# Kernel optimization log

Hardware: AMD Instinct MI355X
Metric: run time of the kernel (lower is better)

## Reference

```python
import jax, jax.numpy as jnp
import numpy as np

SEQ = 21  # fixed by bias parameter shape in the original module

def setup_inputs() -> dict:
    key = jax.random.key(0)
    ks = jax.random.split(key, 6)
    B, H = 8192, 1024
    stdv = 1.0 / np.sqrt(H)
    return {
        "c": jax.random.normal(ks[0], (1, B, H), dtype=jnp.float32),
        "allh": jax.random.normal(ks[1], (SEQ, B, H), dtype=jnp.float32),
        "W": jax.random.uniform(ks[2], (H, H), jnp.float32, -stdv, stdv),
        "V": jax.random.uniform(ks[3], (H, H), jnp.float32, -stdv, stdv),
        "bias": jax.random.uniform(ks[4], (SEQ, H), jnp.float32, -stdv, stdv),
        "Wt": jax.random.uniform(ks[5], (H, 1), jnp.float32, -stdv, stdv),
    }

def reference(c, allh, W, V, bias, Wt):
    # c: [1, B, H] -> [B, 1, H]; allh: [S, B, H] -> [B, S, H]
    c_b = jnp.transpose(c, (1, 0, 2))
    h_b = jnp.transpose(allh, (1, 0, 2))
    wc = jnp.einsum('boh,hk->bok', c_b, W)          # [B, 1, H], broadcasts over S
    vh = jnp.einsum('bsh,hk->bsk', h_b, V)          # [B, S, H]
    e = jnp.tanh(wc + vh + bias)                    # [B, S, H]
    scores = jnp.einsum('bsh,ho->bso', e, Wt)       # [B, S, 1]
    alpha = jax.nn.softmax(scores, axis=1)          # softmax over seq axis
    y = jnp.sum(alpha * h_b, axis=1, keepdims=True) # [B, 1, H]
    return jnp.transpose(y, (1, 0, 2))              # [1, B, H]
```

## Files before the change

kernel.cpp:

```cpp
#include <hip/hip_runtime.h>
#include <hip/hip_bf16.h>
#include <cstdint>
#include <cstddef>

#define Bq 8192
#define Sq 21
#define Hq 1024
#define Mq (Bq * Sq)

typedef __attribute__((ext_vector_type(8))) short short8;
typedef __attribute__((ext_vector_type(4))) float floatx4;

__device__ __forceinline__ short f2b(float x) {
    unsigned u = __builtin_bit_cast(unsigned, x);
    unsigned r = (u + 0x7fffu + ((u >> 16) & 1u)) >> 16;
    return (short)r;
}
__device__ __forceinline__ float b2f(unsigned short b) {
    return __builtin_bit_cast(float, (unsigned)b << 16);
}

__device__ __forceinline__ void gl_lds16(const void* g, void* l) {
    __builtin_amdgcn_global_load_lds(
        (const __attribute__((address_space(1))) unsigned int*)g,
        (__attribute__((address_space(3))) unsigned int*)l, 16, 0, 0);
}

__global__ void transpose_cvt(const float* __restrict__ src,
                              unsigned short* __restrict__ dst) {
    __shared__ float tile[32][33];
    const int n0 = blockIdx.x * 32;
    const int k0 = blockIdx.y * 32;
    const int tx = threadIdx.x;
    const int ty = threadIdx.y;
    #pragma unroll
    for (int i = ty; i < 32; i += 8)
        tile[i][tx] = src[(size_t)(k0 + i) * Hq + n0 + tx];
    __syncthreads();
    #pragma unroll
    for (int i = ty; i < 32; i += 8)
        dst[(size_t)(n0 + i) * Hq + k0 + tx] = (unsigned short)f2b(tile[tx][i]);
}

__global__ __launch_bounds__(256) void cvt_bf16(const float* __restrict__ src,
                                                unsigned short* __restrict__ dst,
                                                int n8) {
    int i = blockIdx.x * 256 + threadIdx.x;
    const int stride = gridDim.x * 256;
    for (; i < n8; i += stride) {
        const float4* s4 = reinterpret_cast<const float4*>(src) + (size_t)i * 2;
        float4 a = s4[0], b = s4[1];
        short8 p;
        p[0] = f2b(a.x); p[1] = f2b(a.y); p[2] = f2b(a.z); p[3] = f2b(a.w);
        p[4] = f2b(b.x); p[5] = f2b(b.y); p[6] = f2b(b.z); p[7] = f2b(b.w);
        reinterpret_cast<short8*>(dst)[i] = p;
    }
}

__global__ __launch_bounds__(256, 3) void gemm_wc2(
    const unsigned short* __restrict__ cb, const unsigned short* __restrict__ Wtr,
    float* __restrict__ wc)
{
    __shared__ unsigned short As[128 * 64];
    __shared__ unsigned short Bs[128 * 64];

    const int n0 = blockIdx.x * 128;
    const int m0 = blockIdx.y * 128;
    const int t = threadIdx.x;
    const int lane = t & 63;
    const int w = t >> 6;

    const int sub = lane >> 3;
    const int k8g = (lane & 7) ^ sub;
    const unsigned short* ap[4];
    const unsigned short* bp[4];
    #pragma unroll
    for (int j = 0; j < 4; ++j) {
        const int r = w * 32 + j * 8 + sub;
        ap[j] = cb + (size_t)(m0 + r) * Hq + k8g * 8;
        bp[j] = Wtr + (size_t)(n0 + r) * Hq + k8g * 8;
    }

    const int wm = (w & 1) * 64;
    const int wn = (w >> 1) * 64;
    const int l15 = lane & 15;
    const int q = lane >> 4;
    const int sw = l15 & 7;

    floatx4 acc[4][4] = {};
    const short8* AsV = (const short8*)As;
    const short8* BsV = (const short8*)Bs;

    for (int k0 = 0; k0 < Hq; k0 += 64) {
        __syncthreads();
        #pragma unroll
        for (int j = 0; j < 4; ++j) {
            gl_lds16(ap[j] + k0, &As[(w * 256 + j * 64) * 8]);
            gl_lds16(bp[j] + k0, &Bs[(w * 256 + j * 64) * 8]);
        }
        __syncthreads();
        #pragma unroll
        for (int kk = 0; kk < 2; ++kk) {
            const int k8 = kk * 4 + q;
            short8 af[4], bfr[4];
            #pragma unroll
            for (int i = 0; i < 4; ++i) {
                af[i]  = AsV[((wm + i * 16 + l15) << 3) | (k8 ^ sw)];
                bfr[i] = BsV[((wn + i * 16 + l15) << 3) | (k8 ^ sw)];
            }
            #pragma unroll
            for (int i = 0; i < 4; ++i)
                #pragma unroll
                for (int j = 0; j < 4; ++j)
                    acc[i][j] = __builtin_amdgcn_mfma_f32_16x16x32_bf16(
                        af[i], bfr[j], acc[i][j], 0, 0, 0);
        }
    }

    #pragma unroll
    for (int i = 0; i < 4; ++i)
        #pragma unroll
        for (int rr = 0; rr < 4; ++rr) {
            const int mm = m0 + wm + i * 16 + q * 4 + rr;
            #pragma unroll
            for (int j = 0; j < 4; ++j) {
                const int nn = n0 + wn + j * 16 + l15;
                wc[(size_t)mm * Hq + nn] = acc[i][j][rr];
            }
        }
}

__global__ __launch_bounds__(256, 3) void gemm_scores2(
    const unsigned short* __restrict__ hb, const unsigned short* __restrict__ Vt,
    const float* __restrict__ wc, const float* __restrict__ bias,
    const float* __restrict__ Wt, float* __restrict__ scores)
{
    __shared__ unsigned short As[128 * 64];
    __shared__ unsigned short Bs[128 * 64];

    const int n0 = blockIdx.x * 128;
    const int m0 = blockIdx.y * 128;
    const int t = threadIdx.x;
    const int lane = t & 63;
    const int w = t >> 6;

    const int sub = lane >> 3;
    const int k8g = (lane & 7) ^ sub;
    const unsigned short* ap[4];
    const unsigned short* bp[4];
    #pragma unroll
    for (int j = 0; j < 4; ++j) {
        const int r = w * 32 + j * 8 + sub;
        const int m = m0 + r;
        const int bb = m / 21;
        const int ss = m - bb * 21;
        ap[j] = hb + ((size_t)ss * Bq + bb) * Hq + k8g * 8;
        bp[j] = Vt + (size_t)(n0 + r) * Hq + k8g * 8;
    }

    const int wm = (w & 1) * 64;
    const int wn = (w >> 1) * 64;
    const int l15 = lane & 15;
    const int q = lane >> 4;
    const int sw = l15 & 7;

    floatx4 acc[4][4] = {};
    const short8* AsV = (const short8*)As;
    const short8* BsV = (const short8*)Bs;

    for (int k0 = 0; k0 < Hq; k0 += 64) {
        __syncthreads();
        #pragma unroll
        for (int j = 0; j < 4; ++j) {
            gl_lds16(ap[j] + k0, &As[(w * 256 + j * 64) * 8]);
            gl_lds16(bp[j] + k0, &Bs[(w * 256 + j * 64) * 8]);
        }
        __syncthreads();
        #pragma unroll
        for (int kk = 0; kk < 2; ++kk) {
            const int k8 = kk * 4 + q;
            short8 af[4], bfr[4];
            #pragma unroll
            for (int i = 0; i < 4; ++i) {
                af[i]  = AsV[((wm + i * 16 + l15) << 3) | (k8 ^ sw)];
                bfr[i] = BsV[((wn + i * 16 + l15) << 3) | (k8 ^ sw)];
            }
            #pragma unroll
            for (int i = 0; i < 4; ++i)
                #pragma unroll
                for (int j = 0; j < 4; ++j)
                    acc[i][j] = __builtin_amdgcn_mfma_f32_16x16x32_bf16(
                        af[i], bfr[j], acc[i][j], 0, 0, 0);
        }
    }

    float wtv[4];
    #pragma unroll
    for (int j = 0; j < 4; ++j) wtv[j] = Wt[n0 + wn + j * 16 + l15];

    #pragma unroll
    for (int i = 0; i < 4; ++i) {
        #pragma unroll
        for (int rr = 0; rr < 4; ++rr) {
            const int mm = m0 + wm + i * 16 + q * 4 + rr;
            const int b2 = mm / 21;
            const int s2 = mm - b2 * 21;
            const float* wcrow = wc + (size_t)b2 * Hq + n0 + wn;
            const float* birow = bias + (size_t)s2 * Hq + n0 + wn;
            float part = 0.f;
            #pragma unroll
            for (int j = 0; j < 4; ++j) {
                const int nl = j * 16 + l15;
                float e = tanhf(acc[i][j][rr] + wcrow[nl] + birow[nl]);
                part += e * wtv[j];
            }
            part += __shfl_xor(part, 1);
            part += __shfl_xor(part, 2);
            part += __shfl_xor(part, 4);
            part += __shfl_xor(part, 8);
            if (l15 == 0) atomicAdd(&scores[mm], part);
        }
    }
}

__global__ __launch_bounds__(256) void softmax_out2(
    const float* __restrict__ scores, const unsigned short* __restrict__ hb,
    float* __restrict__ out)
{
    const int b = blockIdx.x;
    const int t = threadIdx.x;

    float sc[Sq];
    float mx = -1e30f;
    #pragma unroll
    for (int s = 0; s < Sq; ++s) {
        sc[s] = scores[(size_t)b * Sq + s];
        mx = fmaxf(mx, sc[s]);
    }
    float sum = 0.f;
    #pragma unroll
    for (int s = 0; s < Sq; ++s) {
        sc[s] = __expf(sc[s] - mx);
        sum += sc[s];
    }
    const float inv = 1.0f / sum;

    const int h = t * 4;
    float a0 = 0.f, a1 = 0.f, a2 = 0.f, a3 = 0.f;
    #pragma unroll
    for (int s = 0; s < Sq; ++s) {
        const unsigned short* p = hb + ((size_t)s * Bq + b) * Hq + h;
        uint2 u = *reinterpret_cast<const uint2*>(p);
        a0 += sc[s] * b2f((unsigned short)(u.x & 0xffffu));
        a1 += sc[s] * b2f((unsigned short)(u.x >> 16));
        a2 += sc[s] * b2f((unsigned short)(u.y & 0xffffu));
        a3 += sc[s] * b2f((unsigned short)(u.y >> 16));
    }
    float4 r;
    r.x = a0 * inv; r.y = a1 * inv; r.z = a2 * inv; r.w = a3 * inv;
    *reinterpret_cast<float4*>(out + (size_t)b * Hq + h) = r;
}

__global__ __launch_bounds__(256, 2) void gemm_wc_fb(
    const float* __restrict__ c, const unsigned short* __restrict__ Wtr,
    float* __restrict__ wc)
{
    __shared__ short As[128][72];
    __shared__ short Bs[128][72];
    const int m0 = blockIdx.x * 128;
    const int n0 = blockIdx.y * 128;
    const int t = threadIdx.x;
    const int r = t >> 1;
    const int half = t & 1;
    const float*          arow = c + (size_t)(m0 + r) * Hq + half * 32;
    const unsigned short* brow = Wtr + (size_t)(n0 + r) * Hq + half * 32;
    const int lane = t & 63;
    const int w = t >> 6;
    const int wm = (w & 1) * 64;
    const int wn = (w >> 1) * 64;
    const int l15 = lane & 15;
    const int q = lane >> 4;
    floatx4 acc[4][4] = {};
    for (int k0 = 0; k0 < Hq; k0 += 64) {
        __syncthreads();
        const float4* a4 = reinterpret_cast<const float4*>(arow + k0);
        #pragma unroll
        for (int i = 0; i < 4; ++i) {
            float4 v0 = a4[2 * i], v1 = a4[2 * i + 1];
            short8 p;
            p[0] = f2b(v0.x); p[1] = f2b(v0.y); p[2] = f2b(v0.z); p[3] = f2b(v0.w);
            p[4] = f2b(v1.x); p[5] = f2b(v1.y); p[6] = f2b(v1.z); p[7] = f2b(v1.w);
            *reinterpret_cast<short8*>(&As[r][half * 32 + i * 8]) = p;
        }
        const short8* b8 = reinterpret_cast<const short8*>(brow + k0);
        #pragma unroll
        for (int i = 0; i < 4; ++i)
            *reinterpret_cast<short8*>(&Bs[r][half * 32 + i * 8]) = b8[i];
        __syncthreads();
        #pragma unroll
        for (int kk = 0; kk < 64; kk += 32) {
            short8 af[4], bfr[4];
            #pragma unroll
            for (int i = 0; i < 4; ++i)
                af[i] = *reinterpret_cast<const short8*>(&As[wm + i * 16 + l15][kk + q * 8]);
            #pragma unroll
            for (int j = 0; j < 4; ++j)
                bfr[j] = *reinterpret_cast<const short8*>(&Bs[wn + j * 16 + l15][kk + q * 8]);
            #pragma unroll
            for (int i = 0; i < 4; ++i)
                #pragma unroll
                for (int j = 0; j < 4; ++j)
                    acc[i][j] = __builtin_amdgcn_mfma_f32_16x16x32_bf16(
                        af[i], bfr[j], acc[i][j], 0, 0, 0);
        }
    }
    #pragma unroll
    for (int i = 0; i < 4; ++i)
        #pragma unroll
        for (int rr = 0; rr < 4; ++rr) {
            const int mm = m0 + wm + i * 16 + q * 4 + rr;
            #pragma unroll
            for (int j = 0; j < 4; ++j)
                wc[(size_t)mm * Hq + n0 + wn + j * 16 + l15] = acc[i][j][rr];
        }
}

__global__ __launch_bounds__(256, 2) void gemm_scores_fb(
    const float* __restrict__ allh, const unsigned short* __restrict__ Vt,
    const float* __restrict__ wc, const float* __restrict__ bias,
    const float* __restrict__ Wt, float* __restrict__ scores)
{
    __shared__ short As[128][72];
    __shared__ short Bs[128][72];
    const int m0 = blockIdx.x * 128;
    const int n0 = blockIdx.y * 128;
    const int t = threadIdx.x;
    const int r = t >> 1;
    const int half = t & 1;
    const int m = m0 + r;
    const int bb = m / 21;
    const int ss = m - bb * 21;
    const float* arow = allh + (size_t)ss * (Bq * Hq) + (size_t)bb * Hq + half * 32;
    const unsigned short* brow = Vt + (size_t)(n0 + r) * Hq + half * 32;
    const int lane = t & 63;
    const int w = t >> 6;
    const int wm = (w & 1) * 64;
    const int wn = (w >> 1) * 64;
    const int l15 = lane & 15;
    const int q = lane >> 4;
    floatx4 acc[4][4] = {};
    for (int k0 = 0; k0 < Hq; k0 += 64) {
        __syncthreads();
        const float4* a4 = reinterpret_cast<const float4*>(arow + k0);
        #pragma unroll
        for (int i = 0; i < 4; ++i) {
            float4 v0 = a4[2 * i], v1 = a4[2 * i + 1];
            short8 p;
            p[0] = f2b(v0.x); p[1] = f2b(v0.y); p[2] = f2b(v0.z); p[3] = f2b(v0.w);
            p[4] = f2b(v1.x); p[5] = f2b(v1.y); p[6] = f2b(v1.z); p[7] = f2b(v1.w);
            *reinterpret_cast<short8*>(&As[r][half * 32 + i * 8]) = p;
        }
        const short8* b8 = reinterpret_cast<const short8*>(brow + k0);
        #pragma unroll
        for (int i = 0; i < 4; ++i)
            *reinterpret_cast<short8*>(&Bs[r][half * 32 + i * 8]) = b8[i];
        __syncthreads();
        #pragma unroll
        for (int kk = 0; kk < 64; kk += 32) {
            short8 af[4], bfr[4];
            #pragma unroll
            for (int i = 0; i < 4; ++i)
                af[i] = *reinterpret_cast<const short8*>(&As[wm + i * 16 + l15][kk + q * 8]);
            #pragma unroll
            for (int j = 0; j < 4; ++j)
                bfr[j] = *reinterpret_cast<const short8*>(&Bs[wn + j * 16 + l15][kk + q * 8]);
            #pragma unroll
            for (int i = 0; i < 4; ++i)
                #pragma unroll
                for (int j = 0; j < 4; ++j)
                    acc[i][j] = __builtin_amdgcn_mfma_f32_16x16x32_bf16(
                        af[i], bfr[j], acc[i][j], 0, 0, 0);
        }
    }
    float wtv[4];
    #pragma unroll
    for (int j = 0; j < 4; ++j) wtv[j] = Wt[n0 + wn + j * 16 + l15];
    #pragma unroll
    for (int i = 0; i < 4; ++i)
        #pragma unroll
        for (int rr = 0; rr < 4; ++rr) {
            const int mm = m0 + wm + i * 16 + q * 4 + rr;
            const int b2 = mm / 21;
            const int s2 = mm - b2 * 21;
            const float* wcrow = wc + (size_t)b2 * Hq + n0 + wn;
            const float* birow = bias + (size_t)s2 * Hq + n0 + wn;
            float part = 0.f;
            #pragma unroll
            for (int j = 0; j < 4; ++j) {
                const int nl = j * 16 + l15;
                float e = tanhf(acc[i][j][rr] + wcrow[nl] + birow[nl]);
                part += e * wtv[j];
            }
            part += __shfl_xor(part, 1);
            part += __shfl_xor(part, 2);
            part += __shfl_xor(part, 4);
            part += __shfl_xor(part, 8);
            if (l15 == 0) atomicAdd(&scores[mm], part);
        }
}

__global__ __launch_bounds__(256) void softmax_out_fb(
    const float* __restrict__ scores, const float* __restrict__ allh,
    float* __restrict__ out)
{
    const int b = blockIdx.x;
    const int t = threadIdx.x;
    float sc[Sq];
    float mx = -1e30f;
    #pragma unroll
    for (int s = 0; s < Sq; ++s) {
        sc[s] = scores[(size_t)b * Sq + s];
        mx = fmaxf(mx, sc[s]);
    }
    float sum = 0.f;
    #pragma unroll
    for (int s = 0; s < Sq; ++s) {
        sc[s] = __expf(sc[s] - mx);
        sum += sc[s];
    }
    const float inv = 1.0f / sum;
    for (int h = t; h < Hq; h += 256) {
        float acc = 0.f;
        #pragma unroll
        for (int s = 0; s < Sq; ++s)
            acc += sc[s] * allh[(size_t)s * (Bq * Hq) + (size_t)b * Hq + h];
        out[(size_t)b * Hq + h] = acc * inv;
    }
}

extern "C" void kernel_launch(void* const* d_in, const int* in_sizes, int n_in,
                              void* d_out, int out_size, void* d_ws, size_t ws_size,
                              hipStream_t stream) {
    const float* c    = (const float*)d_in[0];
    const float* allh = (const float*)d_in[1];
    const float* W    = (const float*)d_in[2];
    const float* V    = (const float*)d_in[3];
    const float* bias = (const float*)d_in[4];
    const float* Wt   = (const float*)d_in[5];
    float* out = (float*)d_out;
    char* ws = (char*)d_ws;

    const size_t NEED = 411041792ULL;

    if (ws_size >= NEED) {
        unsigned short* Vt  = (unsigned short*)ws;
        unsigned short* Wtr = (unsigned short*)(ws + 2097152);
        float* wc           = (float*)(ws + 4194304);
        float* scores       = (float*)(ws + 37748736);
        unsigned short* cb  = (unsigned short*)(ws + 41943040);
        unsigned short* hb  = (unsigned short*)(ws + 58720256);

        hipMemsetAsync(scores, 0, (size_t)Bq * Sq * sizeof(float), stream);
        transpose_cvt<<<dim3(32, 32), dim3(32, 8), 0, stream>>>(W, Wtr);
        transpose_cvt<<<dim3(32, 32), dim3(32, 8), 0, stream>>>(V, Vt);
        cvt_bf16<<<1024, 256, 0, stream>>>(c, cb, Bq * Hq / 8);
        cvt_bf16<<<4096, 256, 0, stream>>>(allh, hb, Sq * (Bq / 8) * Hq);

        gemm_wc2<<<dim3(Hq / 128, Bq / 128), 256, 0, stream>>>(cb, Wtr, wc);
        gemm_scores2<<<dim3(Hq / 128, Mq / 128), 256, 0, stream>>>(
            hb, Vt, wc, bias, Wt, scores);
        softmax_out2<<<Bq, 256, 0, stream>>>(scores, hb, out);
    } else {
        unsigned short* Vt  = (unsigned short*)ws;
        unsigned short* Wtr = (unsigned short*)(ws + (2u << 20));
        float* wc     = (float*)(ws + (4u << 20));
        float* scores = (float*)(ws + (4u << 20) + (size_t)Bq * Hq * 4);

        hipMemsetAsync(scores, 0, (size_t)Bq * Sq * sizeof(float), stream);
        transpose_cvt<<<dim3(32, 32), dim3(32, 8), 0, stream>>>(W, Wtr);
        transpose_cvt<<<dim3(32, 32), dim3(32, 8), 0, stream>>>(V, Vt);
        gemm_wc_fb<<<dim3(Bq / 128, Hq / 128), 256, 0, stream>>>(c, Wtr, wc);
        gemm_scores_fb<<<dim3(Mq / 128, Hq / 128), 256, 0, stream>>>(
            allh, Vt, wc, bias, Wt, scores);
        softmax_out_fb<<<Bq, 256, 0, stream>>>(scores, allh, out);
    }
}
```

Measured before the change: 1.854 ms.

## Use 256x256 double-buffered tiles with block swizzle and fast tanh in scores GEMM

Replaces the 128x128 scores GEMM with a 256x256 tile, 512-thread kernel where each wave computes 128x64. Global-to-LDS loads are double-buffered so the next K-slice streams in while the current one is multiplied, and the flat grid is swizzled across 8 groups for better L2 locality. tanhf is replaced by an exp/rcp approximation. The larger tile raises register pressure and LDS use (128KB), which limits occupancy, and the fast tanh slightly changes accuracy.

```diff
diff --git a/kernel.cpp b/kernel.cpp
--- a/kernel.cpp
+++ b/kernel.cpp
@@ -18,6 +18,11 @@
 }
 __device__ __forceinline__ float b2f(unsigned short b) {
     return __builtin_bit_cast(float, (unsigned)b << 16);
+}
+
+__device__ __forceinline__ float fast_tanh(float x) {
+    float e = __expf(2.0f * x);
+    return fmaf(-2.0f, __builtin_amdgcn_rcpf(e + 1.0f), 1.0f);
 }
 
 __device__ __forceinline__ void gl_lds16(const void* g, void* l) {
@@ -130,16 +135,57 @@
         }
 }
 
-__global__ __launch_bounds__(256, 3) void gemm_scores2(
+__device__ __forceinline__ void stage_step(
+    unsigned short* __restrict__ buf, int w,
+    const unsigned short* const (&ap)[4], const unsigned short* const (&bp)[4],
+    int k0)
+{
+    unsigned short* dstA = buf + w * 2048;
+    unsigned short* dstB = buf + 16384 + w * 2048;
+    #pragma unroll
+    for (int j = 0; j < 4; ++j) {
+        gl_lds16(ap[j] + k0, dstA + j * 512);
+        gl_lds16(bp[j] + k0, dstB + j * 512);
+    }
+}
+
+__device__ __forceinline__ void compute_step(
+    const unsigned short* __restrict__ buf,
+    floatx4 (&acc)[8][4], int wm, int wn, int l15, int q, int sw)
+{
+    const short8* AsV = (const short8*)buf;
+    const short8* BsV = (const short8*)(buf + 16384);
+    #pragma unroll
+    for (int kk = 0; kk < 2; ++kk) {
+        const int k8 = kk * 4 + q;
+        short8 af[8], bfv[4];
+        #pragma unroll
+        for (int i = 0; i < 8; ++i)
+            af[i] = AsV[((wm + i * 16 + l15) << 3) | (k8 ^ sw)];
+        #pragma unroll
+        for (int j = 0; j < 4; ++j)
+            bfv[j] = BsV[((wn + j * 16 + l15) << 3) | (k8 ^ sw)];
+        #pragma unroll
+        for (int i = 0; i < 8; ++i)
+            #pragma unroll
+            for (int j = 0; j < 4; ++j)
+                acc[i][j] = __builtin_amdgcn_mfma_f32_16x16x32_bf16(
+                    af[i], bfv[j], acc[i][j], 0, 0, 0);
+    }
+}
+
+__global__ __launch_bounds__(512, 2) void gemm_scores256(
     const unsigned short* __restrict__ hb, const unsigned short* __restrict__ Vt,
     const float* __restrict__ wc, const float* __restrict__ bias,
     const float* __restrict__ Wt, float* __restrict__ scores)
 {
-    __shared__ unsigned short As[128 * 64];
-    __shared__ unsigned short Bs[128 * 64];
-
-    const int n0 = blockIdx.x * 128;
-    const int m0 = blockIdx.y * 128;
+    __shared__ unsigned short lds[65536];
+
+    const int orig = blockIdx.x;
+    const int swz = (orig & 7) * 336 + (orig >> 3);
+    const int n0 = (swz & 3) * 256;
+    const int m0 = (swz >> 2) * 256;
+
     const int t = threadIdx.x;
     const int lane = t & 63;
     const int w = t >> 6;
@@ -158,39 +204,31 @@
         bp[j] = Vt + (size_t)(n0 + r) * Hq + k8g * 8;
     }
 
-    const int wm = (w & 1) * 64;
-    const int wn = (w >> 1) * 64;
+    const int wm = (w >> 2) * 128;
+    const int wn = (w & 3) * 64;
     const int l15 = lane & 15;
     const int q = lane >> 4;
     const int sw = l15 & 7;
 
-    floatx4 acc[4][4] = {};
-    const short8* AsV = (const short8*)As;
-    const short8* BsV = (const short8*)Bs;
-
-    for (int k0 = 0; k0 < Hq; k0 += 64) {
-        __syncthreads();
-        #pragma unroll
-        for (int j = 0; j < 4; ++j) {
-            gl_lds16(ap[j] + k0, &As[(w * 256 + j * 64) * 8]);
-            gl_lds16(bp[j] + k0, &Bs[(w * 256 + j * 64) * 8]);
-        }
-        __syncthreads();
-        #pragma unroll
-        for (int kk = 0; kk < 2; ++kk) {
-            const int k8 = kk * 4 + q;
-            short8 af[4], bfr[4];
-            #pragma unroll
-            for (int i = 0; i < 4; ++i) {
-                af[i]  = AsV[((wm + i * 16 + l15) << 3) | (k8 ^ sw)];
-                bfr[i] = BsV[((wn + i * 16 + l15) << 3) | (k8 ^ sw)];
-            }
-            #pragma unroll
-            for (int i = 0; i < 4; ++i)
-                #pragma unroll
-                for (int j = 0; j < 4; ++j)
-                    acc[i][j] = __builtin_amdgcn_mfma_f32_16x16x32_bf16(
-                        af[i], bfr[j], acc[i][j], 0, 0, 0);
+    floatx4 acc[8][4] = {};
+
+    unsigned short* buf0 = lds;
+    unsigned short* buf1 = lds + 32768;
+
+    stage_step(buf0, w, ap, bp, 0);
+    __syncthreads();
+
+    #pragma unroll 1
+    for (int tt = 0; tt < 8; ++tt) {
+        stage_step(buf1, w, ap, bp, tt * 128 + 64);
+        compute_step(buf0, acc, wm, wn, l15, q, sw);
+        __syncthreads();
+        if (tt < 7) {
+            stage_step(buf0, w, ap, bp, tt * 128 + 128);
+            compute_step(buf1, acc, wm, wn, l15, q, sw);
+            __syncthreads();
+        } else {
+            compute_step(buf1, acc, wm, wn, l15, q, sw);
         }
     }
 
@@ -199,7 +237,7 @@
     for (int j = 0; j < 4; ++j) wtv[j] = Wt[n0 + wn + j * 16 + l15];
 
     #pragma unroll
-    for (int i = 0; i < 4; ++i) {
+    for (int i = 0; i < 8; ++i) {
         #pragma unroll
         for (int rr = 0; rr < 4; ++rr) {
             const int mm = m0 + wm + i * 16 + q * 4 + rr;
@@ -211,7 +249,7 @@
             #pragma unroll
             for (int j = 0; j < 4; ++j) {
                 const int nl = j * 16 + l15;
-                float e = tanhf(acc[i][j][rr] + wcrow[nl] + birow[nl]);
+                float e = fast_tanh(acc[i][j][rr] + wcrow[nl] + birow[nl]);
                 part += e * wtv[j];
             }
             part += __shfl_xor(part, 1);
@@ -467,7 +505,7 @@
         cvt_bf16<<<4096, 256, 0, stream>>>(allh, hb, Sq * (Bq / 8) * Hq);
 
         gemm_wc2<<<dim3(Hq / 128, Bq / 128), 256, 0, stream>>>(cb, Wtr, wc);
-        gemm_scores2<<<dim3(Hq / 128, Mq / 128), 256, 0, stream>>>(
+        gemm_scores256<<<dim3((Mq / 256) * (Hq / 256)), dim3(512), 0, stream>>>(
             hb, Vt, wc, bias, Wt, scores);
         softmax_out2<<<Bq, 256, 0, stream>>>(scores, hb, out);
     } else {
```

Result: slower. 3.037 ms (+63.8%).

## Double-buffer LDS in scores GEMM, swizzle block order, use fast tanh

Applied to the files above, without the earlier changes.

The main scores GEMM now uses two LDS buffers so that global-to-LDS loads for the next K tile overlap MFMA compute on the current one, which halves the barriers per tile. The launch becomes a 1D grid whose block index is remapped so that blocks scheduled together share A tiles, aiming at better L2 reuse. The precise tanhf is replaced with an exp/rcp approximation to cut epilogue cost. Doubling LDS use lowers occupancy (launch bounds drop from 3 to 2 blocks per CU), and the fast tanh gives up some accuracy.

```diff
diff --git a/kernel.cpp b/kernel.cpp
--- a/kernel.cpp
+++ b/kernel.cpp
@@ -18,6 +18,11 @@
 }
 __device__ __forceinline__ float b2f(unsigned short b) {
     return __builtin_bit_cast(float, (unsigned)b << 16);
+}
+
+__device__ __forceinline__ float fast_tanh(float x) {
+    float e = __expf(2.0f * x);
+    return fmaf(-2.0f, __builtin_amdgcn_rcpf(e + 1.0f), 1.0f);
 }
 
 __device__ __forceinline__ void gl_lds16(const void* g, void* l) {
@@ -130,16 +135,56 @@
         }
 }
 
-__global__ __launch_bounds__(256, 3) void gemm_scores2(
+__device__ __forceinline__ void stage128(
+    unsigned short* __restrict__ bufA, int w,
+    const unsigned short* const (&ap)[4], const unsigned short* const (&bp)[4],
+    int k0)
+{
+    unsigned short* dstA = bufA + w * 2048;
+    unsigned short* dstB = bufA + 8192 + w * 2048;
+    #pragma unroll
+    for (int j = 0; j < 4; ++j) {
+        gl_lds16(ap[j] + k0, dstA + j * 512);
+        gl_lds16(bp[j] + k0, dstB + j * 512);
+    }
+}
+
+__device__ __forceinline__ void compute128(
+    const unsigned short* __restrict__ bufA,
+    floatx4 (&acc)[4][4], int wm, int wn, int l15, int q, int sw)
+{
+    const short8* AsV = (const short8*)bufA;
+    const short8* BsV = (const short8*)(bufA + 8192);
+    #pragma unroll
+    for (int kk = 0; kk < 2; ++kk) {
+        const int k8 = kk * 4 + q;
+        short8 af[4], bfr[4];
+        #pragma unroll
+        for (int i = 0; i < 4; ++i) {
+            af[i]  = AsV[((wm + i * 16 + l15) << 3) | (k8 ^ sw)];
+            bfr[i] = BsV[((wn + i * 16 + l15) << 3) | (k8 ^ sw)];
+        }
+        #pragma unroll
+        for (int i = 0; i < 4; ++i)
+            #pragma unroll
+            for (int j = 0; j < 4; ++j)
+                acc[i][j] = __builtin_amdgcn_mfma_f32_16x16x32_bf16(
+                    af[i], bfr[j], acc[i][j], 0, 0, 0);
+    }
+}
+
+__global__ __launch_bounds__(256, 2) void gemm_scores128db(
     const unsigned short* __restrict__ hb, const unsigned short* __restrict__ Vt,
     const float* __restrict__ wc, const float* __restrict__ bias,
     const float* __restrict__ Wt, float* __restrict__ scores)
 {
-    __shared__ unsigned short As[128 * 64];
-    __shared__ unsigned short Bs[128 * 64];
-
-    const int n0 = blockIdx.x * 128;
-    const int m0 = blockIdx.y * 128;
+    __shared__ unsigned short lds[32768];
+
+    const int orig = blockIdx.x;
+    const int swz = (orig & 7) * 1344 + (orig >> 3);
+    const int n0 = (swz & 7) * 128;
+    const int m0 = (swz >> 3) * 128;
+
     const int t = threadIdx.x;
     const int lane = t & 63;
     const int w = t >> 6;
@@ -165,32 +210,24 @@
     const int sw = l15 & 7;
 
     floatx4 acc[4][4] = {};
-    const short8* AsV = (const short8*)As;
-    const short8* BsV = (const short8*)Bs;
-
-    for (int k0 = 0; k0 < Hq; k0 += 64) {
-        __syncthreads();
-        #pragma unroll
-        for (int j = 0; j < 4; ++j) {
-            gl_lds16(ap[j] + k0, &As[(w * 256 + j * 64) * 8]);
-            gl_lds16(bp[j] + k0, &Bs[(w * 256 + j * 64) * 8]);
-        }
-        __syncthreads();
-        #pragma unroll
-        for (int kk = 0; kk < 2; ++kk) {
-            const int k8 = kk * 4 + q;
-            short8 af[4], bfr[4];
-            #pragma unroll
-            for (int i = 0; i < 4; ++i) {
-                af[i]  = AsV[((wm + i * 16 + l15) << 3) | (k8 ^ sw)];
-                bfr[i] = BsV[((wn + i * 16 + l15) << 3) | (k8 ^ sw)];
-            }
-            #pragma unroll
-            for (int i = 0; i < 4; ++i)
-                #pragma unroll
-                for (int j = 0; j < 4; ++j)
-                    acc[i][j] = __builtin_amdgcn_mfma_f32_16x16x32_bf16(
-                        af[i], bfr[j], acc[i][j], 0, 0, 0);
+
+    unsigned short* buf0 = lds;
+    unsigned short* buf1 = lds + 16384;
+
+    stage128(buf0, w, ap, bp, 0);
+    __syncthreads();
+
+    #pragma unroll 1
+    for (int tt = 0; tt < 8; ++tt) {
+        stage128(buf1, w, ap, bp, tt * 128 + 64);
+        compute128(buf0, acc, wm, wn, l15, q, sw);
+        __syncthreads();
+        if (tt < 7) {
+            stage128(buf0, w, ap, bp, tt * 128 + 128);
+            compute128(buf1, acc, wm, wn, l15, q, sw);
+            __syncthreads();
+        } else {
+            compute128(buf1, acc, wm, wn, l15, q, sw);
         }
     }
 
@@ -211,7 +248,7 @@
             #pragma unroll
             for (int j = 0; j < 4; ++j) {
                 const int nl = j * 16 + l15;
-                float e = tanhf(acc[i][j][rr] + wcrow[nl] + birow[nl]);
+                float e = fast_tanh(acc[i][j][rr] + wcrow[nl] + birow[nl]);
                 part += e * wtv[j];
             }
             part += __shfl_xor(part, 1);
@@ -467,7 +504,7 @@
         cvt_bf16<<<4096, 256, 0, stream>>>(allh, hb, Sq * (Bq / 8) * Hq);
 
         gemm_wc2<<<dim3(Hq / 128, Bq / 128), 256, 0, stream>>>(cb, Wtr, wc);
-        gemm_scores2<<<dim3(Hq / 128, Mq / 128), 256, 0, stream>>>(
+        gemm_scores128db<<<dim3((Mq / 128) * (Hq / 128)), 256, 0, stream>>>(
             hb, Vt, wc, bias, Wt, scores);
         softmax_out2<<<Bq, 256, 0, stream>>>(scores, hb, out);
     } else {
```

New measurement: 1.725 ms. 1.07x faster.

## Triple-buffer scores GEMM with 512-thread 128x256 tiles and fast tanh

Applied to the files above, without the earlier changes.

Replaces the scores GEMM with a 512-thread block computing 128x256 tiles. Global-to-LDS loads for A and B go through a three-stage LDS ring, so loads for step k+2 are in flight while step k computes, with one barrier per step and MFMA priority raised. It also adds a block-index swizzle for L2 locality and swaps tanhf for an exp/rcp approximation. The risks are one block per CU (lower occupancy), the larger LDS footprint, and slightly lower tanh accuracy.

```diff
diff --git a/kernel.cpp b/kernel.cpp
--- a/kernel.cpp
+++ b/kernel.cpp
@@ -18,6 +18,11 @@
 }
 __device__ __forceinline__ float b2f(unsigned short b) {
     return __builtin_bit_cast(float, (unsigned)b << 16);
+}
+
+__device__ __forceinline__ float fast_tanh(float x) {
+    float e = __expf(2.0f * x);
+    return fmaf(-2.0f, __builtin_amdgcn_rcpf(e + 1.0f), 1.0f);
 }
 
 __device__ __forceinline__ void gl_lds16(const void* g, void* l) {
@@ -130,69 +135,109 @@
         }
 }
 
-__global__ __launch_bounds__(256, 3) void gemm_scores2(
+__device__ __forceinline__ void stage_p3(
+    unsigned short* __restrict__ buf, int w,
+    const unsigned short* const (&gA)[2], const unsigned short* const (&gB)[4],
+    int koff)
+{
+    #pragma unroll
+    for (int c = 0; c < 2; ++c)
+        gl_lds16(gA[c] + koff, buf + c * 4096 + w * 512);
+    #pragma unroll
+    for (int c = 0; c < 4; ++c)
+        gl_lds16(gB[c] + koff, buf + 8192 + c * 4096 + w * 512);
+}
+
+__device__ __forceinline__ void compute_p3(
+    const unsigned short* __restrict__ buf,
+    floatx4 (&acc)[4][4], int wm, int wn, int l15, int q, int sw)
+{
+    const short8* AsV = (const short8*)buf;
+    const short8* BsV = (const short8*)(buf + 8192);
+    #pragma unroll
+    for (int kk = 0; kk < 2; ++kk) {
+        const int k8 = kk * 4 + q;
+        short8 af[4], bfr[4];
+        #pragma unroll
+        for (int i = 0; i < 4; ++i) {
+            af[i]  = AsV[((wm + i * 16 + l15) << 3) | (k8 ^ sw)];
+            bfr[i] = BsV[((wn + i * 16 + l15) << 3) | (k8 ^ sw)];
+        }
+        __builtin_amdgcn_s_setprio(1);
+        #pragma unroll
+        for (int i = 0; i < 4; ++i)
+            #pragma unroll
+            for (int j = 0; j < 4; ++j)
+                acc[i][j] = __builtin_amdgcn_mfma_f32_16x16x32_bf16(
+                    af[i], bfr[j], acc[i][j], 0, 0, 0);
+        __builtin_amdgcn_s_setprio(0);
+    }
+}
+
+__global__ __launch_bounds__(512, 1) void gemm_scores_p3(
     const unsigned short* __restrict__ hb, const unsigned short* __restrict__ Vt,
     const float* __restrict__ wc, const float* __restrict__ bias,
     const float* __restrict__ Wt, float* __restrict__ scores)
 {
-    __shared__ unsigned short As[128 * 64];
-    __shared__ unsigned short Bs[128 * 64];
-
-    const int n0 = blockIdx.x * 128;
-    const int m0 = blockIdx.y * 128;
+    __shared__ unsigned short lds[73728];
+
+    const int orig = blockIdx.x;
+    const int swz = (orig & 7) * 672 + (orig >> 3);
+    const int n0 = (swz & 3) * 256;
+    const int m0 = (swz >> 2) * 128;
+
     const int t = threadIdx.x;
     const int lane = t & 63;
     const int w = t >> 6;
 
-    const int sub = lane >> 3;
-    const int k8g = (lane & 7) ^ sub;
-    const unsigned short* ap[4];
-    const unsigned short* bp[4];
-    #pragma unroll
-    for (int j = 0; j < 4; ++j) {
-        const int r = w * 32 + j * 8 + sub;
-        const int m = m0 + r;
+    const int rr0 = t >> 3;
+    const int csrc = (t & 7) ^ (rr0 & 7);
+    const unsigned short* gA[2];
+    const unsigned short* gB[4];
+    #pragma unroll
+    for (int c = 0; c < 2; ++c) {
+        const int m = m0 + c * 64 + rr0;
         const int bb = m / 21;
         const int ss = m - bb * 21;
-        ap[j] = hb + ((size_t)ss * Bq + bb) * Hq + k8g * 8;
-        bp[j] = Vt + (size_t)(n0 + r) * Hq + k8g * 8;
-    }
-
-    const int wm = (w & 1) * 64;
-    const int wn = (w >> 1) * 64;
+        gA[c] = hb + ((size_t)ss * Bq + bb) * Hq + csrc * 8;
+    }
+    #pragma unroll
+    for (int c = 0; c < 4; ++c)
+        gB[c] = Vt + (size_t)(n0 + c * 64 + rr0) * Hq + csrc * 8;
+
+    const int wm = (w >> 2) * 64;
+    const int wn = (w & 3) * 64;
     const int l15 = lane & 15;
     const int q = lane >> 4;
     const int sw = l15 & 7;
 
     floatx4 acc[4][4] = {};
-    const short8* AsV = (const short8*)As;
-    const short8* BsV = (const short8*)Bs;
-
-    for (int k0 = 0; k0 < Hq; k0 += 64) {
-        __syncthreads();
-        #pragma unroll
-        for (int j = 0; j < 4; ++j) {
-            gl_lds16(ap[j] + k0, &As[(w * 256 + j * 64) * 8]);
-            gl_lds16(bp[j] + k0, &Bs[(w * 256 + j * 64) * 8]);
-        }
-        __syncthreads();
-        #pragma unroll
-        for (int kk = 0; kk < 2; ++kk) {
-            const int k8 = kk * 4 + q;
-            short8 af[4], bfr[4];
-            #pragma unroll
-            for (int i = 0; i < 4; ++i) {
-                af[i]  = AsV[((wm + i * 16 + l15) << 3) | (k8 ^ sw)];
-                bfr[i] = BsV[((wn + i * 16 + l15) << 3) | (k8 ^ sw)];
-            }
-            #pragma unroll
-            for (int i = 0; i < 4; ++i)
-                #pragma unroll
-                for (int j = 0; j < 4; ++j)
-                    acc[i][j] = __builtin_amdgcn_mfma_f32_16x16x32_bf16(
-                        af[i], bfr[j], acc[i][j], 0, 0, 0);
-        }
-    }
+
+    unsigned short* b0 = lds;
+    unsigned short* b1 = lds + 24576;
+    unsigned short* b2 = lds + 49152;
+
+    stage_p3(b0, w, gA, gB, 0);
+    stage_p3(b1, w, gA, gB, 64);
+
+    #pragma unroll 1
+    for (int T = 0; T < 14; ++T) {
+        asm volatile("s_waitcnt vmcnt(6)" ::: "memory");
+        __builtin_amdgcn_s_barrier();
+        __builtin_amdgcn_sched_barrier(0);
+        stage_p3(b2, w, gA, gB, T * 64 + 128);
+        compute_p3(b0, acc, wm, wn, l15, q, sw);
+        unsigned short* tmp = b0; b0 = b1; b1 = b2; b2 = tmp;
+    }
+    asm volatile("s_waitcnt vmcnt(6)" ::: "memory");
+    __builtin_amdgcn_s_barrier();
+    __builtin_amdgcn_sched_barrier(0);
+    compute_p3(b0, acc, wm, wn, l15, q, sw);
+    { unsigned short* tmp = b0; b0 = b1; b1 = b2; b2 = tmp; }
+    asm volatile("s_waitcnt vmcnt(0)" ::: "memory");
+    __builtin_amdgcn_s_barrier();
+    __builtin_amdgcn_sched_barrier(0);
+    compute_p3(b0, acc, wm, wn, l15, q, sw);
 
     float wtv[4];
     #pragma unroll
@@ -203,15 +248,15 @@
         #pragma unroll
         for (int rr = 0; rr < 4; ++rr) {
             const int mm = m0 + wm + i * 16 + q * 4 + rr;
-            const int b2 = mm / 21;
-            const int s2 = mm - b2 * 21;
-            const float* wcrow = wc + (size_t)b2 * Hq + n0 + wn;
+            const int b2i = mm / 21;
+            const int s2 = mm - b2i * 21;
+            const float* wcrow = wc + (size_t)b2i * Hq + n0 + wn;
             const float* birow = bias + (size_t)s2 * Hq + n0 + wn;
             float part = 0.f;
             #pragma unroll
             for (int j = 0; j < 4; ++j) {
                 const int nl = j * 16 + l15;
-                float e = tanhf(acc[i][j][rr] + wcrow[nl] + birow[nl]);
+                float e = fast_tanh(acc[i][j][rr] + wcrow[nl] + birow[nl]);
                 part += e * wtv[j];
             }
             part += __shfl_xor(part, 1);
@@ -467,7 +512,7 @@
         cvt_bf16<<<4096, 256, 0, stream>>>(allh, hb, Sq * (Bq / 8) * Hq);
 
         gemm_wc2<<<dim3(Hq / 128, Bq / 128), 256, 0, stream>>>(cb, Wtr, wc);
-        gemm_scores2<<<dim3(Hq / 128, Mq / 128), 256, 0, stream>>>(
+        gemm_scores_p3<<<dim3((Mq / 128) * (Hq / 256)), dim3(512), 0, stream>>>(
             hb, Vt, wc, bias, Wt, scores);
         softmax_out2<<<Bq, 256, 0, stream>>>(scores, hb, out);
     } else {
```

Measured after the change: 1.647 ms. 1.13x faster.
